# Performance work log

Hardware: AMD Instinct MI355X
Metric: run time of the kernel (lower is better)

## Reference

```python
import jax, jax.numpy as jnp
import numpy as np

NUM_ITERS = 20  # fixed in the original forward: transcribe(dna, iterations=20)


def transcribe(dna_seed, dna_a, dna_b):
    """Fractal DNA decompression: 20 elementwise contractive-map iterations
    over the full weight tensor, starting from the DNA seed."""
    def step(w, ab):
        a, b = ab
        w = a * w + b * jnp.sin(w)
        return w, None
    w, _ = jax.lax.scan(step, dna_seed, (dna_a, dna_b))
    return w  # [out_features, in_features]


def setup_inputs() -> dict:
    key = jax.random.key(0)
    k1, k2, k3, k4, k5 = jax.random.split(key, 5)
    TOKENS, IN_F, OUT_F = 2048, 4096, 4096
    return {
        "x": jax.random.normal(k1, (TOKENS, IN_F), dtype=jnp.float32),
        "dna_seed": jax.random.normal(k2, (OUT_F, IN_F), dtype=jnp.float32),
        "dna_a": jax.random.uniform(k3, (NUM_ITERS,), dtype=jnp.float32),
        "dna_b": jax.random.uniform(k4, (NUM_ITERS,), dtype=jnp.float32),
        "bias": jax.random.normal(k5, (OUT_F,), dtype=jnp.float32),
    }


def reference(x, dna_seed, dna_a, dna_b, bias):
    weight = transcribe(dna_seed, dna_a, dna_b)          # [out, in]
    # F.linear(x, weight, bias) == x @ weight.T + bias
    return jnp.einsum('ti,oi->to', x, weight) + bias     # [tokens, out]
```

## Files before the change

### kernel.cpp

```cpp
#include <hip/hip_runtime.h>

typedef __attribute__((ext_vector_type(8))) short short8;
typedef __attribute__((ext_vector_type(4))) float floatx4;

#define TOKENS 2048
#define IN_F   4096
#define OUT_F  4096
#define NITER  20

#define INV_2PI 0.15915494309189535f
#define TWO_PI  6.283185307179586f

__device__ __forceinline__ unsigned short f2bf(float f) {
    unsigned int u = __builtin_bit_cast(unsigned int, f);
    u += 0x7fffu + ((u >> 16) & 1u);
    return (unsigned short)(u >> 16);
}

__device__ __forceinline__ void step4(float4& v, float a, float bc) {
    v.x = __builtin_fmaf(bc, __builtin_amdgcn_sinf(v.x), a * v.x);
    v.y = __builtin_fmaf(bc, __builtin_amdgcn_sinf(v.y), a * v.y);
    v.z = __builtin_fmaf(bc, __builtin_amdgcn_sinf(v.z), a * v.z);
    v.w = __builtin_fmaf(bc, __builtin_amdgcn_sinf(v.w), a * v.w);
}

#define WBLOCKS (OUT_F * IN_F / 8 / 256)
#define XBLOCKS (TOKENS * IN_F / 8 / 256)

__global__ __launch_bounds__(256) void transcribe_fused_kernel(
    const float4* __restrict__ seed, const float4* __restrict__ xin,
    const float* __restrict__ da, const float* __restrict__ db,
    short8* __restrict__ w_out, short8* __restrict__ x_out)
{
    const int b = blockIdx.x;
    short8 o;
    if (b < WBLOCKS) {
        int i = b * 256 + threadIdx.x;
        float4 u = seed[2 * i];
        float4 v = seed[2 * i + 1];
        u.x *= INV_2PI; u.y *= INV_2PI; u.z *= INV_2PI; u.w *= INV_2PI;
        v.x *= INV_2PI; v.y *= INV_2PI; v.z *= INV_2PI; v.w *= INV_2PI;
#pragma unroll
        for (int t = 0; t < NITER; t++) {
            float a = da[t], bc = db[t] * INV_2PI;
            step4(u, a, bc);
            step4(v, a, bc);
        }
        o[0] = (short)f2bf(u.x * TWO_PI); o[1] = (short)f2bf(u.y * TWO_PI);
        o[2] = (short)f2bf(u.z * TWO_PI); o[3] = (short)f2bf(u.w * TWO_PI);
        o[4] = (short)f2bf(v.x * TWO_PI); o[5] = (short)f2bf(v.y * TWO_PI);
        o[6] = (short)f2bf(v.z * TWO_PI); o[7] = (short)f2bf(v.w * TWO_PI);
        w_out[i] = o;
    } else {
        int i = (b - WBLOCKS) * 256 + threadIdx.x;
        float4 u = xin[2 * i];
        float4 v = xin[2 * i + 1];
        o[0] = (short)f2bf(u.x); o[1] = (short)f2bf(u.y);
        o[2] = (short)f2bf(u.z); o[3] = (short)f2bf(u.w);
        o[4] = (short)f2bf(v.x); o[5] = (short)f2bf(v.y);
        o[6] = (short)f2bf(v.z); o[7] = (short)f2bf(v.w);
        x_out[i] = o;
    }
}

__device__ __forceinline__ void g2l16(const ushort* g, ushort* l) {
    __builtin_amdgcn_global_load_lds(
        (const __attribute__((address_space(1))) unsigned int*)g,
        (__attribute__((address_space(3))) unsigned int*)l, 16, 0, 0);
}

#define BK     64
#define BM     256
#define BN     128
#define NT     (IN_F / BK)
#define ASLOT  (BM * BK)
#define BSLOT  (BN * BK)
#define LDS_BYTES (3 * (ASLOT + BSLOT) * 2)

__global__ __launch_bounds__(512, 2) void gemm_bt_kernel(
    const ushort* __restrict__ A,
    const ushort* __restrict__ B,
    const float* __restrict__ bias,
    float* __restrict__ C)
{
    extern __shared__ ushort lds[];
    ushort* As = lds;
    ushort* Bs = lds + 3 * ASLOT;

    const int tid  = threadIdx.x;
    const int lane = tid & 63;
    const int wid  = tid >> 6;

    const int bid = blockIdx.x;
    const int swz = (bid & 7) * 32 + (bid >> 3);
    const int bn  = swz & 31;
    const int bm  = swz >> 5;

    const int wm = (wid >> 1) << 6;
    const int wn = (wid & 1) << 6;
    const int fm = lane & 15;
    const int q  = lane >> 4;

    const int gcol = (((lane & 7) ^ (lane >> 3)) << 3);

    const ushort* gA = A + (size_t)(bm * BM) * IN_F;
    const ushort* gB = B + (size_t)(bn * BN) * IN_F;

    floatx4 acc[4][4];
#pragma unroll
    for (int i = 0; i < 4; i++)
#pragma unroll
        for (int j = 0; j < 4; j++)
            acc[i][j] = (floatx4){0.f, 0.f, 0.f, 0.f};

#define STAGE(k0v, sl)                                                        \
    {                                                                         \
        _Pragma("unroll")                                                     \
        for (int u = 0; u < 4; u++) {                                         \
            const int cb = ((u << 3) | wid) << 6;                             \
            const int r  = (cb >> 3) + (lane >> 3);                           \
            g2l16(gA + (size_t)r * IN_F + (k0v) + gcol,                       \
                  As + (sl) * ASLOT + cb * 8 + lane * 8);                     \
        }                                                                     \
        _Pragma("unroll")                                                     \
        for (int u = 0; u < 2; u++) {                                         \
            const int cb = ((u << 3) | wid) << 6;                             \
            const int r  = (cb >> 3) + (lane >> 3);                           \
            g2l16(gB + (size_t)r * IN_F + (k0v) + gcol,                       \
                  Bs + (sl) * BSLOT + cb * 8 + lane * 8);                     \
        }                                                                     \
    }

#define LOADFRAG(s_, sl)                                                      \
    const int sa = (((q + 4 * (s_)) & 7) ^ (fm & 7)) << 3;                    \
    _Pragma("unroll")                                                         \
    for (int i = 0; i < 4; i++) {                                             \
        af[i] = *(const short8*)(As + (sl) * ASLOT + (wm + i * 16 + fm) * BK + sa); \
        bf[i] = *(const short8*)(Bs + (sl) * BSLOT + (wn + i * 16 + fm) * BK + sa); \
    }

#define MFMA16()                                                              \
    __builtin_amdgcn_s_setprio(1);                                            \
    _Pragma("unroll")                                                         \
    for (int i = 0; i < 4; i++)                                               \
        _Pragma("unroll")                                                     \
        for (int j = 0; j < 4; j++)                                           \
            acc[i][j] = __builtin_amdgcn_mfma_f32_16x16x32_bf16(              \
                af[i], bf[j], acc[i][j], 0, 0, 0);                            \
    __builtin_amdgcn_s_setprio(0);

#define TILE_MAIN(vm, sl, k3)                                                 \
    {                                                                         \
        asm volatile("s_waitcnt vmcnt(" #vm ")" ::: "memory");                \
        __builtin_amdgcn_s_barrier();                                         \
        {                                                                     \
            short8 af[4], bf[4];                                              \
            LOADFRAG(0, sl);                                                  \
            MFMA16();                                                         \
        }                                                                     \
        {                                                                     \
            short8 af[4], bf[4];                                              \
            LOADFRAG(1, sl);                                                  \
            asm volatile("s_waitcnt lgkmcnt(0)" ::: "memory");                \
            __builtin_amdgcn_s_barrier();                                     \
            STAGE(k3, sl);                                                    \
            __builtin_amdgcn_sched_barrier(0);                                \
            MFMA16();                                                         \
        }                                                                     \
    }

#define TILE_TAIL(vm, sl)                                                     \
    {                                                                         \
        asm volatile("s_waitcnt vmcnt(" #vm ")" ::: "memory");                \
        __builtin_amdgcn_s_barrier();                                         \
        {                                                                     \
            short8 af[4], bf[4];                                              \
            LOADFRAG(0, sl);                                                  \
            MFMA16();                                                         \
        }                                                                     \
        {                                                                     \
            short8 af[4], bf[4];                                              \
            LOADFRAG(1, sl);                                                  \
            MFMA16();                                                         \
        }                                                                     \
    }

    STAGE(0 * BK, 0);
    STAGE(1 * BK, 1);
    STAGE(2 * BK, 2);

    int st   = 0;
    int kpre = 3 * BK;
#pragma unroll 1
    for (int t = 0; t <= NT - 4; ++t) {
        TILE_MAIN(12, st, kpre);
        kpre += BK;
        st = (st == 2) ? 0 : st + 1;
    }
    TILE_TAIL(12, 1);
    TILE_TAIL(6, 2);
    TILE_TAIL(0, 0);

#undef STAGE
#undef LOADFRAG
#undef MFMA16
#undef TILE_MAIN
#undef TILE_TAIL

    const int cn = lane & 15;
    const int cm = (lane >> 4) << 2;
    float bv[4];
#pragma unroll
    for (int j = 0; j < 4; j++)
        bv[j] = bias[bn * BN + wn + j * 16 + cn];
#pragma unroll
    for (int i = 0; i < 4; i++) {
#pragma unroll
        for (int r = 0; r < 4; r++) {
            int m = bm * BM + wm + i * 16 + cm + r;
            float* crow = C + (size_t)m * OUT_F + bn * BN + wn + cn;
#pragma unroll
            for (int j = 0; j < 4; j++)
                crow[j * 16] = acc[i][j][r] + bv[j];
        }
    }
}

extern "C" void kernel_launch(void* const* d_in, const int* in_sizes, int n_in,
                              void* d_out, int out_size, void* d_ws, size_t ws_size,
                              hipStream_t stream) {
    const float* x    = (const float*)d_in[0];
    const float* seed = (const float*)d_in[1];
    const float* da   = (const float*)d_in[2];
    const float* db   = (const float*)d_in[3];
    const float* bias = (const float*)d_in[4];
    float* out        = (float*)d_out;

    ushort* w_bf = (ushort*)d_ws;
    ushort* x_bf = w_bf + (size_t)OUT_F * IN_F;

    static bool lds_attr_set = false;
    if (!lds_attr_set) {
        hipFuncSetAttribute(reinterpret_cast<const void*>(gemm_bt_kernel),
                            hipFuncAttributeMaxDynamicSharedMemorySize,
                            LDS_BYTES);
        lds_attr_set = true;
    }

    transcribe_fused_kernel<<<WBLOCKS + XBLOCKS, 256, 0, stream>>>(
        (const float4*)seed, (const float4*)x, da, db,
        (short8*)w_bf, (short8*)x_bf);

    gemm_bt_kernel<<<dim3(32 * 8), dim3(512), LDS_BYTES, stream>>>(
        x_bf, w_bf, bias, out);
}
```

Baseline: 207.4 us.

## Split K across two wave groups with larger per-wave tiles and LDS reduction

Each wave now computes a 128x64 output sub-tile, and the eight waves form two groups that each handle half of every K tile (the s_=0 or s_=1 fragment). Partial sums are combined through LDS at the end, and group 0 adds the bias and writes the output. The goal is fewer LDS fragment reads per MFMA (better register reuse) and one barrier-pair per tile instead of two sub-steps. The block-to-tile swizzle also changes. The cost is double the accumulator registers (128 floats), which can spill or reduce occupancy under launch_bounds(512,2), plus an extra LDS reduction epilogue.

New measurement: 216.6 us. 1.04x slower.

```diff
diff --git a/kernel.cpp b/kernel.cpp
--- a/kernel.cpp
+++ b/kernel.cpp
@@ -90,25 +90,26 @@
     const int tid  = threadIdx.x;
     const int lane = tid & 63;
     const int wid  = tid >> 6;
+    const int g    = wid >> 2;
+    const int w2   = wid & 3;
+    const int wm   = (w2 >> 1) << 7;
+    const int wn   = (w2 & 1) << 6;
+    const int fm   = lane & 15;
+    const int q    = lane >> 4;
 
     const int bid = blockIdx.x;
-    const int swz = (bid & 7) * 32 + (bid >> 3);
-    const int bn  = swz & 31;
-    const int bm  = swz >> 5;
-
-    const int wm = (wid >> 1) << 6;
-    const int wn = (wid & 1) << 6;
-    const int fm = lane & 15;
-    const int q  = lane >> 4;
+    const int jj  = bid >> 3;
+    const int bn  = (bid & 7) * 4 + (jj & 3);
+    const int bm  = jj >> 2;
 
     const int gcol = (((lane & 7) ^ (lane >> 3)) << 3);
 
     const ushort* gA = A + (size_t)(bm * BM) * IN_F;
     const ushort* gB = B + (size_t)(bn * BN) * IN_F;
 
-    floatx4 acc[4][4];
-#pragma unroll
-    for (int i = 0; i < 4; i++)
+    floatx4 acc[8][4];
+#pragma unroll
+    for (int i = 0; i < 8; i++)
 #pragma unroll
         for (int j = 0; j < 4; j++)
             acc[i][j] = (floatx4){0.f, 0.f, 0.f, 0.f};
@@ -131,18 +132,19 @@
         }                                                                     \
     }
 
-#define LOADFRAG(s_, sl)                                                      \
-    const int sa = (((q + 4 * (s_)) & 7) ^ (fm & 7)) << 3;                    \
+#define LOADFRAG(sl)                                                          \
+    const int sa = (((q + 4 * g) & 7) ^ (fm & 7)) << 3;                       \
     _Pragma("unroll")                                                         \
-    for (int i = 0; i < 4; i++) {                                             \
+    for (int i = 0; i < 8; i++)                                               \
         af[i] = *(const short8*)(As + (sl) * ASLOT + (wm + i * 16 + fm) * BK + sa); \
-        bf[i] = *(const short8*)(Bs + (sl) * BSLOT + (wn + i * 16 + fm) * BK + sa); \
-    }
-
-#define MFMA16()                                                              \
+    _Pragma("unroll")                                                         \
+    for (int j = 0; j < 4; j++)                                               \
+        bf[j] = *(const short8*)(Bs + (sl) * BSLOT + (wn + j * 16 + fm) * BK + sa);
+
+#define MFMA32()                                                              \
     __builtin_amdgcn_s_setprio(1);                                            \
     _Pragma("unroll")                                                         \
-    for (int i = 0; i < 4; i++)                                               \
+    for (int i = 0; i < 8; i++)                                               \
         _Pragma("unroll")                                                     \
         for (int j = 0; j < 4; j++)                                           \
             acc[i][j] = __builtin_amdgcn_mfma_f32_16x16x32_bf16(              \
@@ -153,36 +155,22 @@
     {                                                                         \
         asm volatile("s_waitcnt vmcnt(" #vm ")" ::: "memory");                \
         __builtin_amdgcn_s_barrier();                                         \
-        {                                                                     \
-            short8 af[4], bf[4];                                              \
-            LOADFRAG(0, sl);                                                  \
-            MFMA16();                                                         \
-        }                                                                     \
-        {                                                                     \
-            short8 af[4], bf[4];                                              \
-            LOADFRAG(1, sl);                                                  \
-            asm volatile("s_waitcnt lgkmcnt(0)" ::: "memory");                \
-            __builtin_amdgcn_s_barrier();                                     \
-            STAGE(k3, sl);                                                    \
-            __builtin_amdgcn_sched_barrier(0);                                \
-            MFMA16();                                                         \
-        }                                                                     \
+        short8 af[8], bf[4];                                                  \
+        LOADFRAG(sl);                                                         \
+        asm volatile("s_waitcnt lgkmcnt(0)" ::: "memory");                    \
+        __builtin_amdgcn_s_barrier();                                         \
+        STAGE(k3, sl);                                                        \
+        __builtin_amdgcn_sched_barrier(0);                                    \
+        MFMA32();                                                             \
     }
 
 #define TILE_TAIL(vm, sl)                                                     \
     {                                                                         \
         asm volatile("s_waitcnt vmcnt(" #vm ")" ::: "memory");                \
         __builtin_amdgcn_s_barrier();                                         \
-        {                                                                     \
-            short8 af[4], bf[4];                                              \
-            LOADFRAG(0, sl);                                                  \
-            MFMA16();                                                         \
-        }                                                                     \
-        {                                                                     \
-            short8 af[4], bf[4];                                              \
-            LOADFRAG(1, sl);                                                  \
-            MFMA16();                                                         \
-        }                                                                     \
+        short8 af[8], bf[4];                                                  \
+        LOADFRAG(sl);                                                         \
+        MFMA32();                                                             \
     }
 
     STAGE(0 * BK, 0);
@@ -203,25 +191,43 @@
 
 #undef STAGE
 #undef LOADFRAG
-#undef MFMA16
+#undef MFMA32
 #undef TILE_MAIN
 #undef TILE_TAIL
 
-    const int cn = lane & 15;
-    const int cm = (lane >> 4) << 2;
-    float bv[4];
-#pragma unroll
-    for (int j = 0; j < 4; j++)
-        bv[j] = bias[bn * BN + wn + j * 16 + cn];
-#pragma unroll
-    for (int i = 0; i < 4; i++) {
-#pragma unroll
-        for (int r = 0; r < 4; r++) {
-            int m = bm * BM + wm + i * 16 + cm + r;
-            float* crow = C + (size_t)m * OUT_F + bn * BN + wn + cn;
+    __syncthreads();
+    floatx4* red = (floatx4*)lds;
+    if (g == 1) {
+#pragma unroll
+        for (int i = 0; i < 8; i++)
 #pragma unroll
             for (int j = 0; j < 4; j++)
-                crow[j * 16] = acc[i][j][r] + bv[j];
+                red[(size_t)(w2 * 32 + i * 4 + j) * 64 + lane] = acc[i][j];
+    }
+    __syncthreads();
+    if (g == 0) {
+        const int cn = lane & 15;
+        const int cm = (lane >> 4) << 2;
+        float bv[4];
+#pragma unroll
+        for (int j = 0; j < 4; j++)
+            bv[j] = bias[bn * BN + wn + j * 16 + cn];
+#pragma unroll
+        for (int i = 0; i < 8; i++) {
+#pragma unroll
+            for (int j = 0; j < 4; j++) {
+                floatx4 p = red[(size_t)(w2 * 32 + i * 4 + j) * 64 + lane];
+#pragma unroll
+                for (int r = 0; r < 4; r++) acc[i][j][r] += p[r];
+            }
+#pragma unroll
+            for (int r = 0; r < 4; r++) {
+                int m = bm * BM + wm + i * 16 + cm + r;
+                float* crow = C + (size_t)m * OUT_F + bn * BN + wn + cn;
+#pragma unroll
+                for (int j = 0; j < 4; j++)
+                    crow[j * 16] = acc[i][j][r] + bv[j];
+            }
         }
     }
 }
```
